# Optimization experiments

Measured on AMD Instinct MI355X. Metric: run time of the kernel, lower is better.

The kernel has to match this reference:

```python
import jax, jax.numpy as jnp
import numpy as np

# Real Clebsch-Gordan for 1o x 1o -> 2e: orthonormal symmetric-traceless basis
# (matches e3nn component-normalized tensor_product up to basis-sign convention).
_s2 = 1.0 / np.sqrt(2.0)
_s6 = 1.0 / np.sqrt(6.0)
_CG2 = np.zeros((5, 3, 3), np.float32)
_CG2[0, 0, 1] = _CG2[0, 1, 0] = _s2          # xy
_CG2[1, 1, 2] = _CG2[1, 2, 1] = _s2          # yz
_CG2[2, 0, 0] = -_s6; _CG2[2, 1, 1] = -_s6; _CG2[2, 2, 2] = 2 * _s6  # 2z^2-x^2-y^2
_CG2[3, 0, 2] = _CG2[3, 2, 0] = _s2          # xz
_CG2[4, 0, 0] = _s2; _CG2[4, 1, 1] = -_s2    # x^2-y^2
CG2 = jnp.asarray(_CG2)

DEN = 16.0   # denominator init kwarg
EPS = 1e-9


def setup_inputs() -> dict:
    key = jax.random.key(0)
    ks = jax.random.split(key, 16)
    N, E, C = 10000, 160000, 32
    def w(k, fi, fo):
        # e3nn Linear: N(0,1) weights with 1/sqrt(fan_in) path normalization (folded in).
        return jax.random.normal(k, (fi, fo), dtype=jnp.float32) / jnp.sqrt(float(fi))
    return {
        "node_0e": jax.random.normal(ks[0], (N, C), dtype=jnp.float32),
        "node_1o": jax.random.normal(ks[1], (N, C, 3), dtype=jnp.float32),
        "positions": jax.random.normal(ks[2], (N, 3), dtype=jnp.float32),
        "senders": jax.random.randint(ks[3], (E,), 0, N, dtype=jnp.int32),
        "receivers": jax.random.randint(ks[4], (E,), 0, N, dtype=jnp.int32),
        "W_pre_0e": w(ks[5], 2 * C, C),
        "W_pre_1o": w(ks[6], 2 * C, C),
        "W_pre_2e": w(ks[7], C, C),
        "W_post_0e": w(ks[8], C, C),
        "W_post_1o": w(ks[9], C, C),
        "W_post_2e": w(ks[10], C, C),
        "W_sc_0e": w(ks[11], C, C),
        "W_sc_1o": w(ks[12], C, C),
    }


def reference(node_0e, node_1o, positions, senders, receivers,
              W_pre_0e, W_pre_1o, W_pre_2e,
              W_post_0e, W_post_1o, W_post_2e,
              W_sc_0e, W_sc_1o):
    N = positions.shape[0]
    # --- edge update: spherical harmonics (lmax=1, normalize=True, component norm) ---
    rel = positions[receivers] - positions[senders]                       # [E,3]
    sh = jnp.sqrt(3.0) * rel / jnp.maximum(
        jnp.linalg.norm(rel, axis=-1, keepdims=True), EPS)                # 1x1o, [E,3]
    x0 = node_0e[senders]                                                 # [E,C]
    x1 = node_1o[senders]                                                 # [E,C,3]
    # full tensor product sender (x) sh
    tp_1o = x0[:, :, None] * sh[:, None, :]                               # 0e x 1o -> 1o
    tp_0e = jnp.einsum('eci,ei->ec', x1, sh) / jnp.sqrt(3.0)              # 1o x 1o -> 0e
    tp_1e = jnp.cross(x1, sh[:, None, :]) / jnp.sqrt(2.0)                 # 1o x 1o -> 1e
    tp_2e = jnp.einsum('eci,ej,mij->ecm', x1, sh, CG2)                    # 1o x 1o -> 2e
    # message = concatenate([sender, tp]).regroup()
    m0 = jnp.concatenate([x0, tp_0e], axis=1)                             # [E,2C]  0e
    m1 = jnp.concatenate([x1, tp_1o], axis=1)                             # [E,2C,3] 1o
    # --- jraph aggregation: scatter-sum edges into receivers ---
    a0 = jax.ops.segment_sum(m0, receivers, num_segments=N) / DEN         # [N,2C]
    a1 = jax.ops.segment_sum(m1, receivers, num_segments=N) / DEN         # [N,2C,3]
    a2 = jax.ops.segment_sum(tp_2e, receivers, num_segments=N) / DEN      # [N,C,5]
    _ = jax.ops.segment_sum(tp_1e, receivers, num_segments=N)             # 1e dropped by linear_pre (not in target irreps)
    # --- node update ---
    h0 = jax.nn.gelu(a0 @ W_pre_0e)                                       # scalar_activation on 0e only
    h1 = jnp.einsum('nci,cd->ndi', a1, W_pre_1o)
    h2 = jnp.einsum('ncm,cd->ndm', a2, W_pre_2e)
    o0 = h0 @ W_post_0e + node_0e @ W_sc_0e
    o1 = jnp.einsum('nci,cd->ndi', h1, W_post_1o) + jnp.einsum('nci,cd->ndi', node_1o, W_sc_1o)
    o2 = jnp.einsum('ncm,cd->ndm', h2, W_post_2e)  # shortcut 2e block is zero (force_irreps_out)
    return jnp.concatenate([o0, o1.reshape(N, -1), o2.reshape(N, -1)], axis=1)  # [N, 32+96+160]
```

## Files before the change

### kernel.cpp

```cpp
#include <hip/hip_runtime.h>
#include <math.h>

#define C 32
#define OUT_DIM 288
#define MAXDEG 64
#define AGG_ROWS 17
#define AGG_S (AGG_ROWS * 32)

typedef __attribute__((ext_vector_type(8))) short short8v;
typedef __attribute__((ext_vector_type(4))) float float4v;

__device__ __forceinline__ float4v mfma_bf16(short8v a, short8v b, float4v c) {
    return __builtin_amdgcn_mfma_f32_16x16x32_bf16(a, b, c, 0, 0, 0);
}

__device__ __forceinline__ unsigned short f2b(float x) {
    unsigned int u = __float_as_uint(x);
    u = u + 0x7FFFu + ((u >> 16) & 1u);
    return (unsigned short)(u >> 16);
}

__device__ __forceinline__ float gelu_tanh(float x) {
    float x3 = x * x * x;
    float t = tanhf(0.7978845608028654f * (x + 0.044715f * x3));
    return 0.5f * x * (1.0f + t);
}

__global__ void zero_kernel(int* __restrict__ p, int n) {
    int i = blockIdx.x * 256 + threadIdx.x;
    if (i < n) p[i] = 0;
}

__global__ void wprep_kernel(const float* __restrict__ Wpre0,
                             const float* __restrict__ Wpre1,
                             const float* __restrict__ Wpre2,
                             const float* __restrict__ Wpost0,
                             const float* __restrict__ Wpost1,
                             const float* __restrict__ Wpost2,
                             const float* __restrict__ Wsc0,
                             const float* __restrict__ Wsc1,
                             unsigned short* __restrict__ wt) {
    const int b = blockIdx.x;
    const float* src;
    switch (b) {
        case 0: src = Wpre0;        break;
        case 1: src = Wpre0 + 1024; break;
        case 2: src = Wpre1;        break;
        case 3: src = Wpre1 + 1024; break;
        case 4: src = Wpre2;        break;
        case 5: src = Wpost0;       break;
        case 6: src = Wpost1;       break;
        case 7: src = Wpost2;       break;
        case 8: src = Wsc0;         break;
        default: src = Wsc1;        break;
    }
    unsigned short* dst = wt + b * 1024;
    for (int i = threadIdx.x; i < 1024; i += 256) {
        const int cc = i >> 5, dd = i & 31;
        dst[dd * 32 + cc] = f2b(src[cc * 32 + dd]);
    }
}

__global__ void scatter_sh_kernel(const int* __restrict__ recv,
                                  const int* __restrict__ senders,
                                  const float* __restrict__ pos, int E,
                                  int* __restrict__ counts, float4* __restrict__ adj) {
    int e = blockIdx.x * 256 + threadIdx.x;
    if (e < E) {
        const int r = recv[e];
        const int s = senders[e];
        const float rx = pos[r * 3 + 0] - pos[s * 3 + 0];
        const float ry = pos[r * 3 + 1] - pos[s * 3 + 1];
        const float rz = pos[r * 3 + 2] - pos[s * 3 + 2];
        const float nrm = sqrtf(rx * rx + ry * ry + rz * rz);
        const float f = 1.7320508075688772f / fmaxf(nrm, 1e-9f);
        const int p = atomicAdd(&counts[r], 1);
        if (p < MAXDEG)
            adj[(size_t)r * MAXDEG + p] = make_float4(rx * f, ry * f, rz * f, __int_as_float(s));
    }
}

__global__ __launch_bounds__(256) void edge_agg_kernel(
    const float* __restrict__ node0, const float* __restrict__ node1,
    const int* __restrict__ counts, const float4* __restrict__ adj,
    unsigned short* __restrict__ aggb, int N)
{
    __shared__ float prt[2][2][13][32];

    const int tid     = threadIdx.x;
    const int wv      = tid >> 6;
    const int slot    = wv >> 1;
    const int portion = wv & 1;
    const int lane    = tid & 63;
    const int half    = lane >> 5;
    const int c       = lane & 31;
    const int node    = blockIdx.x * 2 + slot;
    const bool valid  = (node < N);

    const float S2 = 0.70710678118654752f;
    const float S6 = 0.40824829046386302f;
    const float INV_SQRT3 = 0.57735026918962576f;
    const float INV_DEN = 1.0f / 16.0f;

    float ax0 = 0.f, atp0 = 0.f;
    float ax1x = 0.f, ax1y = 0.f, ax1z = 0.f;
    float at1x = 0.f, at1y = 0.f, at1z = 0.f;
    float a2v0 = 0.f, a2v1 = 0.f, a2v2 = 0.f, a2v3 = 0.f, a2v4 = 0.f;

#define EDGE_ACC(A, X0, U1)                                                 \
    {                                                                       \
        const float shx = (A).x, shy = (A).y, shz = (A).z;                  \
        ax0 += (X0);                                                        \
        atp0 += (U1).x * shx + (U1).y * shy + (U1).z * shz;                 \
        ax1x += (U1).x; ax1y += (U1).y; ax1z += (U1).z;                     \
        at1x += (X0) * shx; at1y += (X0) * shy; at1z += (X0) * shz;         \
        a2v0 += (U1).x * shy + (U1).y * shx;                                \
        a2v1 += (U1).y * shz + (U1).z * shy;                                \
        a2v2 += 2.f * (U1).z * shz - (U1).x * shx - (U1).y * shy;           \
        a2v3 += (U1).x * shz + (U1).z * shx;                                \
        a2v4 += (U1).x * shx - (U1).y * shy;                                \
    }

    if (valid) {
        const int deg = min(counts[node], MAXDEG);
        const int beg = node * MAXDEG;
        const int end = beg + deg;
        int k = beg + portion * 2 + half;
        while (k + 4 < end) {
            const float4 A0 = adj[k];
            const float4 A1 = adj[k + 4];
            const int b0 = __float_as_int(A0.w) * C + c;
            const int b1 = __float_as_int(A1.w) * C + c;
            const float q0 = node0[b0];
            const float q1 = node0[b1];
            const float3 u0 = *(const float3*)(node1 + b0 * 3);
            const float3 u1 = *(const float3*)(node1 + b1 * 3);
            EDGE_ACC(A0, q0, u0);
            EDGE_ACC(A1, q1, u1);
            k += 8;
        }
        if (k < end) {
            const float4 A0 = adj[k];
            const int b0 = __float_as_int(A0.w) * C + c;
            const float q0 = node0[b0];
            const float3 u0 = *(const float3*)(node1 + b0 * 3);
            EDGE_ACC(A0, q0, u0);
        }
    }
#undef EDGE_ACC

    ax0  += __shfl_xor(ax0, 32, 64);
    atp0 += __shfl_xor(atp0, 32, 64);
    ax1x += __shfl_xor(ax1x, 32, 64);
    ax1y += __shfl_xor(ax1y, 32, 64);
    ax1z += __shfl_xor(ax1z, 32, 64);
    at1x += __shfl_xor(at1x, 32, 64);
    at1y += __shfl_xor(at1y, 32, 64);
    at1z += __shfl_xor(at1z, 32, 64);
    a2v0 += __shfl_xor(a2v0, 32, 64);
    a2v1 += __shfl_xor(a2v1, 32, 64);
    a2v2 += __shfl_xor(a2v2, 32, 64);
    a2v3 += __shfl_xor(a2v3, 32, 64);
    a2v4 += __shfl_xor(a2v4, 32, 64);

    if (half == 0) {
        float* p = &prt[slot][portion][0][c];
        p[0 * 32]  = ax0;
        p[1 * 32]  = atp0;
        p[2 * 32]  = ax1x;
        p[3 * 32]  = ax1y;
        p[4 * 32]  = ax1z;
        p[5 * 32]  = at1x;
        p[6 * 32]  = at1y;
        p[7 * 32]  = at1z;
        p[8 * 32]  = a2v0;
        p[9 * 32]  = a2v1;
        p[10 * 32] = a2v2;
        p[11 * 32] = a2v3;
        p[12 * 32] = a2v4;
    }
    __syncthreads();

    if (valid) {
        unsigned short* ag = aggb + (size_t)node * AGG_S + c;
        const float SA = INV_DEN;
        const float SB = INV_DEN * INV_SQRT3;
        const float S2D = S2 * INV_DEN;
        const float S6D = S6 * INV_DEN;
#define PRT(j) (prt[slot][0][j][c] + prt[slot][1][j][c])
        if (portion == 0) {
            if (half == 0) {
                ag[0 * 32] = f2b(PRT(0) * SA);
                ag[1 * 32] = f2b(PRT(1) * SB);
                ag[2 * 32] = f2b(PRT(2) * SA);
                ag[3 * 32] = f2b(PRT(3) * SA);
                ag[4 * 32] = f2b(PRT(4) * SA);
                ag[5 * 32] = f2b(PRT(5) * SA);
                ag[6 * 32] = f2b(PRT(6) * SA);
            } else {
                ag[7 * 32]  = f2b(PRT(7) * SA);
                ag[8 * 32]  = f2b(PRT(8) * S2D);
                ag[9 * 32]  = f2b(PRT(9) * S2D);
                ag[10 * 32] = f2b(PRT(10) * S6D);
                ag[11 * 32] = f2b(PRT(11) * S2D);
                ag[12 * 32] = f2b(PRT(12) * S2D);
            }
        } else {
            if (half == 0) {
                const float x0n = node0[node * C + c];
                const float x1x = node1[(node * C + c) * 3 + 0];
                ag[13 * 32] = f2b(x0n);
                ag[14 * 32] = f2b(x1x);
            } else {
                const float x1y = node1[(node * C + c) * 3 + 1];
                const float x1z = node1[(node * C + c) * 3 + 2];
                ag[15 * 32] = f2b(x1y);
                ag[16 * 32] = f2b(x1z);
            }
        }
#undef PRT
    }
}

__global__ __launch_bounds__(256) void node_mfma_kernel(
    const unsigned short* __restrict__ aggb,
    const unsigned short* __restrict__ wt,
    float* __restrict__ out, int N, int ntiles)
{
    __shared__ unsigned short tr[4][16][48];

    const int wv   = threadIdx.x >> 6;
    const int wave = blockIdx.x * 4 + wv;
    const int tile = __builtin_amdgcn_readfirstlane(wave / 9);
    const int t    = __builtin_amdgcn_readfirstlane(wave % 9);
    if (tile >= ntiles) return;

    const int lane = threadIdx.x & 63;
    const int r    = lane & 15;
    const int kg   = lane >> 4;
    const int k0   = kg * 8;

    const unsigned short *pb1, *pb2 = nullptr, *qb1, *qb2 = nullptr;
    int rowA1, rowA2 = -1, rowX = -1, obase, ostride;
    if (t == 0) {
        rowA1 = 0; rowA2 = 1; rowX = 13;
        pb1 = wt + 0 * 1024; pb2 = wt + 1 * 1024;
        qb1 = wt + 5 * 1024; qb2 = wt + 8 * 1024;
        obase = 0; ostride = 1;
    } else if (t <= 3) {
        const int i = t - 1;
        rowA1 = 2 + i; rowA2 = 5 + i; rowX = 14 + i;
        pb1 = wt + 2 * 1024; pb2 = wt + 3 * 1024;
        qb1 = wt + 6 * 1024; qb2 = wt + 9 * 1024;
        obase = 32 + i; ostride = 3;
    } else {
        const int m = t - 4;
        rowA1 = 8 + m;
        pb1 = wt + 4 * 1024; qb1 = wt + 7 * 1024;
        obase = 128 + m; ostride = 5;
    }

    short8v bp1[2], bp2[2], bq1[2], bq2[2];
#pragma unroll
    for (int dt = 0; dt < 2; ++dt) {
        const int d = dt * 16 + r;
        bp1[dt] = *(const short8v*)(pb1 + d * 32 + k0);
        bq1[dt] = *(const short8v*)(qb1 + d * 32 + k0);
    }
    if (rowA2 >= 0) {
#pragma unroll
        for (int dt = 0; dt < 2; ++dt) {
            const int d = dt * 16 + r;
            bp2[dt] = *(const short8v*)(pb2 + d * 32 + k0);
            bq2[dt] = *(const short8v*)(qb2 + d * 32 + k0);
        }
    }

    const int node = tile * 16 + r;
    const int nclamp = node < N ? node : (N - 1);
    const unsigned short* ap = aggb + (size_t)nclamp * AGG_S;

    float4v acc0 = {0.f, 0.f, 0.f, 0.f};
    float4v acc1 = {0.f, 0.f, 0.f, 0.f};
    {
        const short8v a1 = *(const short8v*)(ap + rowA1 * 32 + k0);
        acc0 = mfma_bf16(a1, bp1[0], acc0);
        acc1 = mfma_bf16(a1, bp1[1], acc1);
    }
    if (rowA2 >= 0) {
        const short8v a2 = *(const short8v*)(ap + rowA2 * 32 + k0);
        acc0 = mfma_bf16(a2, bp2[0], acc0);
        acc1 = mfma_bf16(a2, bp2[1], acc1);
    }
    if (t == 0) {
#pragma unroll
        for (int q = 0; q < 4; ++q) {
            acc0[q] = gelu_tanh(acc0[q]);
            acc1[q] = gelu_tanh(acc1[q]);
        }
    }

#pragma unroll
    for (int q = 0; q < 4; ++q) {
        tr[wv][kg * 4 + q][r]      = f2b(acc0[q]);
        tr[wv][kg * 4 + q][16 + r] = f2b(acc1[q]);
    }
    asm volatile("s_waitcnt lgkmcnt(0)" ::: "memory");
    __builtin_amdgcn_sched_barrier(0);

    const short8v ha = *(const short8v*)&tr[wv][r][k0];
    float4v o0 = {0.f, 0.f, 0.f, 0.f};
    float4v o1 = {0.f, 0.f, 0.f, 0.f};
    o0 = mfma_bf16(ha, bq1[0], o0);
    o1 = mfma_bf16(ha, bq1[1], o1);
    if (rowX >= 0) {
        const short8v xa = *(const short8v*)(ap + rowX * 32 + k0);
        o0 = mfma_bf16(xa, bq2[0], o0);
        o1 = mfma_bf16(xa, bq2[1], o1);
    }

#pragma unroll
    for (int q = 0; q < 4; ++q) {
        const int nodeo = tile * 16 + kg * 4 + q;
        if (nodeo < N) {
            float* po = out + (size_t)nodeo * OUT_DIM + obase;
            po[r * ostride]        = o0[q];
            po[(16 + r) * ostride] = o1[q];
        }
    }
}

extern "C" void kernel_launch(void* const* d_in, const int* in_sizes, int n_in,
                              void* d_out, int out_size, void* d_ws, size_t ws_size,
                              hipStream_t stream) {
    const float* node0   = (const float*)d_in[0];
    const float* node1   = (const float*)d_in[1];
    const float* pos     = (const float*)d_in[2];
    const int*   senders = (const int*)d_in[3];
    const int*   recv    = (const int*)d_in[4];
    const float* Wpre0   = (const float*)d_in[5];
    const float* Wpre1   = (const float*)d_in[6];
    const float* Wpre2   = (const float*)d_in[7];
    const float* Wpost0  = (const float*)d_in[8];
    const float* Wpost1  = (const float*)d_in[9];
    const float* Wpost2  = (const float*)d_in[10];
    const float* Wsc0    = (const float*)d_in[11];
    const float* Wsc1    = (const float*)d_in[12];
    float* out = (float*)d_out;

    const int N = in_sizes[2] / 3;
    const int E = in_sizes[3];

    int* counts = (int*)d_ws;
    size_t adj_off = ((size_t)N * sizeof(int) + 15) & ~(size_t)15;
    float4* adj = (float4*)((char*)d_ws + adj_off);
    unsigned short* aggb = (unsigned short*)((char*)d_ws + adj_off + (size_t)N * MAXDEG * sizeof(float4));
    unsigned short* wt = aggb + (size_t)N * AGG_S;

    wprep_kernel<<<10, 256, 0, stream>>>(
        Wpre0, Wpre1, Wpre2, Wpost0, Wpost1, Wpost2, Wsc0, Wsc1, wt);
    zero_kernel<<<(N + 255) / 256, 256, 0, stream>>>(counts, N);
    scatter_sh_kernel<<<(E + 255) / 256, 256, 0, stream>>>(recv, senders, pos, E, counts, adj);
    edge_agg_kernel<<<(N + 1) / 2, 256, 0, stream>>>(node0, node1, counts, adj, aggb, N);

    const int ntiles = (N + 15) / 16;
    const int nwaves = ntiles * 9;
    node_mfma_kernel<<<(nwaves + 3) / 4, 256, 0, stream>>>(
        aggb, wt, out, N, ntiles);
}
```

Measured before the change: 52.43 us.

## Fuse edge aggregation with node MFMA linears via shared-memory staging

```diff
diff --git a/kernel.cpp b/kernel.cpp
--- a/kernel.cpp
+++ b/kernel.cpp
@@ -4,8 +4,7 @@
 #define C 32
 #define OUT_DIM 288
 #define MAXDEG 64
-#define AGG_ROWS 17
-#define AGG_S (AGG_ROWS * 32)
+#define AGG_PAD 552
 
 typedef __attribute__((ext_vector_type(8))) short short8v;
 typedef __attribute__((ext_vector_type(4))) float float4v;
@@ -26,38 +25,39 @@
     return 0.5f * x * (1.0f + t);
 }
 
-__global__ void zero_kernel(int* __restrict__ p, int n) {
-    int i = blockIdx.x * 256 + threadIdx.x;
-    if (i < n) p[i] = 0;
-}
-
-__global__ void wprep_kernel(const float* __restrict__ Wpre0,
-                             const float* __restrict__ Wpre1,
-                             const float* __restrict__ Wpre2,
-                             const float* __restrict__ Wpost0,
-                             const float* __restrict__ Wpost1,
-                             const float* __restrict__ Wpost2,
-                             const float* __restrict__ Wsc0,
-                             const float* __restrict__ Wsc1,
-                             unsigned short* __restrict__ wt) {
+__global__ void wprep_zero_kernel(const float* __restrict__ Wpre0,
+                                  const float* __restrict__ Wpre1,
+                                  const float* __restrict__ Wpre2,
+                                  const float* __restrict__ Wpost0,
+                                  const float* __restrict__ Wpost1,
+                                  const float* __restrict__ Wpost2,
+                                  const float* __restrict__ Wsc0,
+                                  const float* __restrict__ Wsc1,
+                                  unsigned short* __restrict__ wt,
+                                  int* __restrict__ counts, int N) {
     const int b = blockIdx.x;
-    const float* src;
-    switch (b) {
-        case 0: src = Wpre0;        break;
-        case 1: src = Wpre0 + 1024; break;
-        case 2: src = Wpre1;        break;
-        case 3: src = Wpre1 + 1024; break;
-        case 4: src = Wpre2;        break;
-        case 5: src = Wpost0;       break;
-        case 6: src = Wpost1;       break;
-        case 7: src = Wpost2;       break;
-        case 8: src = Wsc0;         break;
-        default: src = Wsc1;        break;
-    }
-    unsigned short* dst = wt + b * 1024;
-    for (int i = threadIdx.x; i < 1024; i += 256) {
-        const int cc = i >> 5, dd = i & 31;
-        dst[dd * 32 + cc] = f2b(src[cc * 32 + dd]);
+    if (b < 10) {
+        const float* src;
+        switch (b) {
+            case 0: src = Wpre0;        break;
+            case 1: src = Wpre0 + 1024; break;
+            case 2: src = Wpre1;        break;
+            case 3: src = Wpre1 + 1024; break;
+            case 4: src = Wpre2;        break;
+            case 5: src = Wpost0;       break;
+            case 6: src = Wpost1;       break;
+            case 7: src = Wpost2;       break;
+            case 8: src = Wsc0;         break;
+            default: src = Wsc1;        break;
+        }
+        unsigned short* dst = wt + b * 1024;
+        for (int i = threadIdx.x; i < 1024; i += 256) {
+            const int cc = i >> 5, dd = i & 31;
+            dst[dd * 32 + cc] = f2b(src[cc * 32 + dd]);
+        }
+    } else {
+        const int i = (b - 10) * 256 + threadIdx.x;
+        if (i < N) counts[i] = 0;
     }
 }
 
@@ -72,30 +72,31 @@
         const float rx = pos[r * 3 + 0] - pos[s * 3 + 0];
         const float ry = pos[r * 3 + 1] - pos[s * 3 + 1];
         const float rz = pos[r * 3 + 2] - pos[s * 3 + 2];
-        const float nrm = sqrtf(rx * rx + ry * ry + rz * rz);
-        const float f = 1.7320508075688772f / fmaxf(nrm, 1e-9f);
+        const float d2 = rx * rx + ry * ry + rz * rz;
+        const float f = 1.7320508075688772f * rsqrtf(fmaxf(d2, 1e-18f));
         const int p = atomicAdd(&counts[r], 1);
         if (p < MAXDEG)
             adj[(size_t)r * MAXDEG + p] = make_float4(rx * f, ry * f, rz * f, __int_as_float(s));
     }
 }
 
-__global__ __launch_bounds__(256) void edge_agg_kernel(
+__global__ __launch_bounds__(1024) void fused_node_kernel(
     const float* __restrict__ node0, const float* __restrict__ node1,
     const int* __restrict__ counts, const float4* __restrict__ adj,
-    unsigned short* __restrict__ aggb, int N)
+    const unsigned short* __restrict__ wt,
+    float* __restrict__ out, int N)
 {
-    __shared__ float prt[2][2][13][32];
-
-    const int tid     = threadIdx.x;
-    const int wv      = tid >> 6;
-    const int slot    = wv >> 1;
-    const int portion = wv & 1;
-    const int lane    = tid & 63;
-    const int half    = lane >> 5;
-    const int c       = lane & 31;
-    const int node    = blockIdx.x * 2 + slot;
-    const bool valid  = (node < N);
+    __shared__ unsigned short aggs[16 * AGG_PAD];
+    __shared__ unsigned short tr[9][16][48];
+
+    const int tid  = threadIdx.x;
+    const int w    = tid >> 6;
+    const int lane = tid & 63;
+    const int half = lane >> 5;
+    const int c    = lane & 31;
+    const int tile = blockIdx.x;
+    const int node = tile * 16 + w;
+    const bool valid = (node < N);
 
     const float S2 = 0.70710678118654752f;
     const float S6 = 0.40824829046386302f;
@@ -125,10 +126,10 @@
         const int deg = min(counts[node], MAXDEG);
         const int beg = node * MAXDEG;
         const int end = beg + deg;
-        int k = beg + portion * 2 + half;
-        while (k + 4 < end) {
+        int k = beg + half;
+        while (k + 2 < end) {
             const float4 A0 = adj[k];
-            const float4 A1 = adj[k + 4];
+            const float4 A1 = adj[k + 2];
             const int b0 = __float_as_int(A0.w) * C + c;
             const int b1 = __float_as_int(A1.w) * C + c;
             const float q0 = node0[b0];
@@ -137,7 +138,7 @@
             const float3 u1 = *(const float3*)(node1 + b1 * 3);
             EDGE_ACC(A0, q0, u0);
             EDGE_ACC(A1, q1, u1);
-            k += 8;
+            k += 4;
         }
         if (k < end) {
             const float4 A0 = adj[k];
@@ -163,169 +164,121 @@
     a2v3 += __shfl_xor(a2v3, 32, 64);
     a2v4 += __shfl_xor(a2v4, 32, 64);
 
-    if (half == 0) {
-        float* p = &prt[slot][portion][0][c];
-        p[0 * 32]  = ax0;
-        p[1 * 32]  = atp0;
-        p[2 * 32]  = ax1x;
-        p[3 * 32]  = ax1y;
-        p[4 * 32]  = ax1z;
-        p[5 * 32]  = at1x;
-        p[6 * 32]  = at1y;
-        p[7 * 32]  = at1z;
-        p[8 * 32]  = a2v0;
-        p[9 * 32]  = a2v1;
-        p[10 * 32] = a2v2;
-        p[11 * 32] = a2v3;
-        p[12 * 32] = a2v4;
-    }
-    __syncthreads();
-
-    if (valid) {
-        unsigned short* ag = aggb + (size_t)node * AGG_S + c;
+    {
+        const int nfeat = valid ? node : 0;
+        const float x0n = node0[nfeat * C + c];
+        const float3 xu = *(const float3*)(node1 + (nfeat * C + c) * 3);
+        unsigned short* ag = aggs + w * AGG_PAD + c;
         const float SA = INV_DEN;
         const float SB = INV_DEN * INV_SQRT3;
         const float S2D = S2 * INV_DEN;
         const float S6D = S6 * INV_DEN;
-#define PRT(j) (prt[slot][0][j][c] + prt[slot][1][j][c])
-        if (portion == 0) {
-            if (half == 0) {
-                ag[0 * 32] = f2b(PRT(0) * SA);
-                ag[1 * 32] = f2b(PRT(1) * SB);
-                ag[2 * 32] = f2b(PRT(2) * SA);
-                ag[3 * 32] = f2b(PRT(3) * SA);
-                ag[4 * 32] = f2b(PRT(4) * SA);
-                ag[5 * 32] = f2b(PRT(5) * SA);
-                ag[6 * 32] = f2b(PRT(6) * SA);
-            } else {
-                ag[7 * 32]  = f2b(PRT(7) * SA);
-                ag[8 * 32]  = f2b(PRT(8) * S2D);
-                ag[9 * 32]  = f2b(PRT(9) * S2D);
-                ag[10 * 32] = f2b(PRT(10) * S6D);
-                ag[11 * 32] = f2b(PRT(11) * S2D);
-                ag[12 * 32] = f2b(PRT(12) * S2D);
+        if (half == 0) {
+            ag[0 * 32]  = f2b(ax0 * SA);
+            ag[1 * 32]  = f2b(atp0 * SB);
+            ag[2 * 32]  = f2b(ax1x * SA);
+            ag[3 * 32]  = f2b(ax1y * SA);
+            ag[4 * 32]  = f2b(ax1z * SA);
+            ag[5 * 32]  = f2b(at1x * SA);
+            ag[6 * 32]  = f2b(at1y * SA);
+            ag[13 * 32] = f2b(x0n);
+            ag[14 * 32] = f2b(xu.x);
+        } else {
+            ag[7 * 32]  = f2b(at1z * SA);
+            ag[8 * 32]  = f2b(a2v0 * S2D);
+            ag[9 * 32]  = f2b(a2v1 * S2D);
+            ag[10 * 32] = f2b(a2v2 * S6D);
+            ag[11 * 32] = f2b(a2v3 * S2D);
+            ag[12 * 32] = f2b(a2v4 * S2D);
+            ag[15 * 32] = f2b(xu.y);
+            ag[16 * 32] = f2b(xu.z);
+        }
+    }
+    __syncthreads();
+
+    if (w < 9) {
+        const int t  = w;
+        const int r  = lane & 15;
+        const int kg = lane >> 4;
+        const int k0 = kg * 8;
+
+        const unsigned short *pb1, *pb2 = nullptr, *qb1, *qb2 = nullptr;
+        int rowA1, rowA2 = -1, rowX = -1, obase, ostride;
+        if (t == 0) {
+            rowA1 = 0; rowA2 = 1; rowX = 13;
+            pb1 = wt + 0 * 1024; pb2 = wt + 1 * 1024;
+            qb1 = wt + 5 * 1024; qb2 = wt + 8 * 1024;
+            obase = 0; ostride = 1;
+        } else if (t <= 3) {
+            const int i = t - 1;
+            rowA1 = 2 + i; rowA2 = 5 + i; rowX = 14 + i;
+            pb1 = wt + 2 * 1024; pb2 = wt + 3 * 1024;
+            qb1 = wt + 6 * 1024; qb2 = wt + 9 * 1024;
+            obase = 32 + i; ostride = 3;
+        } else {
+            const int m = t - 4;
+            rowA1 = 8 + m;
+            pb1 = wt + 4 * 1024; qb1 = wt + 7 * 1024;
+            obase = 128 + m; ostride = 5;
+        }
+
+        const unsigned short* ap = aggs + r * AGG_PAD;
+
+        float4v acc0 = {0.f, 0.f, 0.f, 0.f};
+        float4v acc1 = {0.f, 0.f, 0.f, 0.f};
+        {
+            const short8v a1 = *(const short8v*)(ap + rowA1 * 32 + k0);
+            const short8v bp1a = *(const short8v*)(pb1 + (0 * 16 + r) * 32 + k0);
+            const short8v bp1b = *(const short8v*)(pb1 + (1 * 16 + r) * 32 + k0);
+            acc0 = mfma_bf16(a1, bp1a, acc0);
+            acc1 = mfma_bf16(a1, bp1b, acc1);
+        }
+        if (rowA2 >= 0) {
+            const short8v a2 = *(const short8v*)(ap + rowA2 * 32 + k0);
+            const short8v bp2a = *(const short8v*)(pb2 + (0 * 16 + r) * 32 + k0);
+            const short8v bp2b = *(const short8v*)(pb2 + (1 * 16 + r) * 32 + k0);
+            acc0 = mfma_bf16(a2, bp2a, acc0);
+            acc1 = mfma_bf16(a2, bp2b, acc1);
+        }
+        if (t == 0) {
+#pragma unroll
+            for (int q = 0; q < 4; ++q) {
+                acc0[q] = gelu_tanh(acc0[q]);
+                acc1[q] = gelu_tanh(acc1[q]);
             }
-        } else {
-            if (half == 0) {
-                const float x0n = node0[node * C + c];
-                const float x1x = node1[(node * C + c) * 3 + 0];
-                ag[13 * 32] = f2b(x0n);
-                ag[14 * 32] = f2b(x1x);
-            } else {
-                const float x1y = node1[(node * C + c) * 3 + 1];
-                const float x1z = node1[(node * C + c) * 3 + 2];
-                ag[15 * 32] = f2b(x1y);
-                ag[16 * 32] = f2b(x1z);
-            }
-        }
-#undef PRT
-    }
-}
-
-__global__ __launch_bounds__(256) void node_mfma_kernel(
-    const unsigned short* __restrict__ aggb,
-    const unsigned short* __restrict__ wt,
-    float* __restrict__ out, int N, int ntiles)
-{
-    __shared__ unsigned short tr[4][16][48];
-
-    const int wv   = threadIdx.x >> 6;
-    const int wave = blockIdx.x * 4 + wv;
-    const int tile = __builtin_amdgcn_readfirstlane(wave / 9);
-    const int t    = __builtin_amdgcn_readfirstlane(wave % 9);
-    if (tile >= ntiles) return;
-
-    const int lane = threadIdx.x & 63;
-    const int r    = lane & 15;
-    const int kg   = lane >> 4;
-    const int k0   = kg * 8;
-
-    const unsigned short *pb1, *pb2 = nullptr, *qb1, *qb2 = nullptr;
-    int rowA1, rowA2 = -1, rowX = -1, obase, ostride;
-    if (t == 0) {
-        rowA1 = 0; rowA2 = 1; rowX = 13;
-        pb1 = wt + 0 * 1024; pb2 = wt + 1 * 1024;
-        qb1 = wt + 5 * 1024; qb2 = wt + 8 * 1024;
-        obase = 0; ostride = 1;
-    } else if (t <= 3) {
-        const int i = t - 1;
-        rowA1 = 2 + i; rowA2 = 5 + i; rowX = 14 + i;
-        pb1 = wt + 2 * 1024; pb2 = wt + 3 * 1024;
-        qb1 = wt + 6 * 1024; qb2 = wt + 9 * 1024;
-        obase = 32 + i; ostride = 3;
-    } else {
-        const int m = t - 4;
-        rowA1 = 8 + m;
-        pb1 = wt + 4 * 1024; qb1 = wt + 7 * 1024;
-        obase = 128 + m; ostride = 5;
-    }
-
-    short8v bp1[2], bp2[2], bq1[2], bq2[2];
-#pragma unroll
-    for (int dt = 0; dt < 2; ++dt) {
-        const int d = dt * 16 + r;
-        bp1[dt] = *(const short8v*)(pb1 + d * 32 + k0);
-        bq1[dt] = *(const short8v*)(qb1 + d * 32 + k0);
-    }
-    if (rowA2 >= 0) {
-#pragma unroll
-        for (int dt = 0; dt < 2; ++dt) {
-            const int d = dt * 16 + r;
-            bp2[dt] = *(const short8v*)(pb2 + d * 32 + k0);
-            bq2[dt] = *(const short8v*)(qb2 + d * 32 + k0);
-        }
-    }
-
-    const int node = tile * 16 + r;
-    const int nclamp = node < N ? node : (N - 1);
-    const unsigned short* ap = aggb + (size_t)nclamp * AGG_S;
-
-    float4v acc0 = {0.f, 0.f, 0.f, 0.f};
-    float4v acc1 = {0.f, 0.f, 0.f, 0.f};
-    {
-        const short8v a1 = *(const short8v*)(ap + rowA1 * 32 + k0);
-        acc0 = mfma_bf16(a1, bp1[0], acc0);
-        acc1 = mfma_bf16(a1, bp1[1], acc1);
-    }
-    if (rowA2 >= 0) {
-        const short8v a2 = *(const short8v*)(ap + rowA2 * 32 + k0);
-        acc0 = mfma_bf16(a2, bp2[0], acc0);
-        acc1 = mfma_bf16(a2, bp2[1], acc1);
-    }
-    if (t == 0) {
+        }
+
 #pragma unroll
         for (int q = 0; q < 4; ++q) {
-            acc0[q] = gelu_tanh(acc0[q]);
-            acc1[q] = gelu_tanh(acc1[q]);
-        }
-    }
+            tr[w][kg * 4 + q][r]      = f2b(acc0[q]);
+            tr[w][kg * 4 + q][16 + r] = f2b(acc1[q]);
+        }
+        asm volatile("s_waitcnt lgkmcnt(0)" ::: "memory");
+        __builtin_amdgcn_sched_barrier(0);
+
+        const short8v ha = *(const short8v*)&tr[w][r][k0];
+        const short8v bq1a = *(const short8v*)(qb1 + (0 * 16 + r) * 32 + k0);
+        const short8v bq1b = *(const short8v*)(qb1 + (1 * 16 + r) * 32 + k0);
+        float4v o0 = {0.f, 0.f, 0.f, 0.f};
+        float4v o1 = {0.f, 0.f, 0.f, 0.f};
+        o0 = mfma_bf16(ha, bq1a, o0);
+        o1 = mfma_bf16(ha, bq1b, o1);
+        if (rowX >= 0) {
+            const short8v xa = *(const short8v*)(ap + rowX * 32 + k0);
+            const short8v bq2a = *(const short8v*)(qb2 + (0 * 16 + r) * 32 + k0);
+            const short8v bq2b = *(const short8v*)(qb2 + (1 * 16 + r) * 32 + k0);
+            o0 = mfma_bf16(xa, bq2a, o0);
+            o1 = mfma_bf16(xa, bq2b, o1);
+        }
 
 #pragma unroll
-    for (int q = 0; q < 4; ++q) {
-        tr[wv][kg * 4 + q][r]      = f2b(acc0[q]);
-        tr[wv][kg * 4 + q][16 + r] = f2b(acc1[q]);
-    }
-    asm volatile("s_waitcnt lgkmcnt(0)" ::: "memory");
-    __builtin_amdgcn_sched_barrier(0);
-
-    const short8v ha = *(const short8v*)&tr[wv][r][k0];
-    float4v o0 = {0.f, 0.f, 0.f, 0.f};
-    float4v o1 = {0.f, 0.f, 0.f, 0.f};
-    o0 = mfma_bf16(ha, bq1[0], o0);
-    o1 = mfma_bf16(ha, bq1[1], o1);
-    if (rowX >= 0) {
-        const short8v xa = *(const short8v*)(ap + rowX * 32 + k0);
-        o0 = mfma_bf16(xa, bq2[0], o0);
-        o1 = mfma_bf16(xa, bq2[1], o1);
-    }
-
-#pragma unroll
-    for (int q = 0; q < 4; ++q) {
-        const int nodeo = tile * 16 + kg * 4 + q;
-        if (nodeo < N) {
-            float* po = out + (size_t)nodeo * OUT_DIM + obase;
-            po[r * ostride]        = o0[q];
-            po[(16 + r) * ostride] = o1[q];
+        for (int q = 0; q < 4; ++q) {
+            const int nodeo = tile * 16 + kg * 4 + q;
+            if (nodeo < N) {
+                float* po = out + (size_t)nodeo * OUT_DIM + obase;
+                po[r * ostride]        = o0[q];
+                po[(16 + r) * ostride] = o1[q];
+            }
         }
     }
 }
@@ -354,17 +307,14 @@
     int* counts = (int*)d_ws;
     size_t adj_off = ((size_t)N * sizeof(int) + 15) & ~(size_t)15;
     float4* adj = (float4*)((char*)d_ws + adj_off);
-    unsigned short* aggb = (unsigned short*)((char*)d_ws + adj_off + (size_t)N * MAXDEG * sizeof(float4));
-    unsigned short* wt = aggb + (size_t)N * AGG_S;
-
-    wprep_kernel<<<10, 256, 0, stream>>>(
-        Wpre0, Wpre1, Wpre2, Wpost0, Wpost1, Wpost2, Wsc0, Wsc1, wt);
-    zero_kernel<<<(N + 255) / 256, 256, 0, stream>>>(counts, N);
+    unsigned short* wt = (unsigned short*)((char*)d_ws + adj_off + (size_t)N * MAXDEG * sizeof(float4));
+
+    const int zero_blocks = (N + 255) / 256;
+    wprep_zero_kernel<<<10 + zero_blocks, 256, 0, stream>>>(
+        Wpre0, Wpre1, Wpre2, Wpost0, Wpost1, Wpost2, Wsc0, Wsc1, wt, counts, N);
     scatter_sh_kernel<<<(E + 255) / 256, 256, 0, stream>>>(recv, senders, pos, E, counts, adj);
-    edge_agg_kernel<<<(N + 1) / 2, 256, 0, stream>>>(node0, node1, counts, adj, aggb, N);
 
     const int ntiles = (N + 15) / 16;
-    const int nwaves = ntiles * 9;
-    node_mfma_kernel<<<(nwaves + 3) / 4, 256, 0, stream>>>(
-        aggb, wt, out, N, ntiles);
-}
+    fused_node_kernel<<<ntiles, 1024, 0, stream>>>(
+        node0, node1, counts, adj, wt, out, N);
+}
```

Measured after the change: 44.27 us (median of 2 runs). -15.6%, faster.
